# Optimization experiments

Hardware: AMD Instinct MI355X
Metric: run time of the kernel (lower is better)

## Reference

```python
import jax, jax.numpy as jnp
import numpy as np

R, C, N, E = 1, 4, 10000, 160000
H, EF, L, OUT = 128, 16, 3, 64


def _gelu(v):
    # torch F.gelu default = exact erf gelu
    return jax.nn.gelu(v, approximate=False)


def setup_inputs() -> dict:
    key = jax.random.key(0)
    ks = jax.random.split(key, 16)
    s = 0.05
    return {
        "x": jax.random.normal(ks[0], (R, C, N, H), jnp.float32),
        "node_mask": jax.random.uniform(ks[1], (R, C, N, 1), jnp.float32),
        "edge_attr": jax.random.normal(ks[2], (E, EF), jnp.float32),
        "bondW": jax.random.normal(ks[3], (EF, H), jnp.float32) * s,
        "bondb": jnp.zeros((H,), jnp.float32),
        "convW1": jax.random.normal(ks[4], (L, H, H), jnp.float32) * s,
        "convb1": jnp.zeros((L, H), jnp.float32),
        "convW2": jax.random.normal(ks[5], (L, H, H), jnp.float32) * s,
        "convb2": jnp.zeros((L, H), jnp.float32),
        "eps": jnp.zeros((L,), jnp.float32),
        "mlpW1": jax.random.normal(ks[6], (H, H), jnp.float32) * s,
        "mlpb1": jnp.zeros((H,), jnp.float32),
        "mlpW2": jax.random.normal(ks[7], (H, OUT), jnp.float32) * s,
        "mlpb2": jnp.zeros((OUT,), jnp.float32),
        "edge_index": jax.random.randint(ks[8], (2, E), 0, N, jnp.int32),
        "batch": jnp.zeros((N,), jnp.int32),
    }


def reference(x, node_mask, edge_attr, bondW, bondb, convW1, convb1, convW2, convb2,
              eps, mlpW1, mlpb1, mlpW2, mlpb2, edge_index, batch):
    src, dst = edge_index[0], edge_index[1]
    # shared bond encoder (Linear), broadcast to [1,1,E,H]
    edge_emb = edge_attr @ bondW + bondb                      # [E, H]
    # edge_weight = node_mask gathered at both endpoints      # [R, C, E, 1]
    edge_mask = node_mask[:, :, src, :] * node_mask[:, :, dst, :]
    for l in range(L):
        # gather-add-GELU-weight-scatter message passing
        msg = _gelu(x[:, :, src, :] + edge_emb) * edge_mask   # [R, C, E, H]
        agg = jnp.zeros_like(x).at[:, :, dst, :].add(msg)     # scatter_sum over dst
        h = (1.0 + eps[l]) * x + agg
        # conv mlp: Linear -> GELU -> Linear
        h = _gelu(h @ convW1[l] + convb1[l]) @ convW2[l] + convb2[l]
        h = _gelu(h)  # outer activation (norm=Identity, dropout=0)
        x = x + h     # residual
    # final MLP (num_mlp_layers=2, PyG MLP default relu act)
    y = jax.nn.relu(x @ mlpW1 + mlpb1) @ mlpW2 + mlpb2        # [R, C, N, OUT]
    denom = jax.lax.stop_gradient(node_mask).sum(axis=2)      # [R, C, 1]
    out = (y * node_mask).sum(axis=2) / denom                 # [R, C, OUT]
    return out
```

## Files before the change

kernel.cpp:

```cpp
#include <hip/hip_runtime.h>
#include <hip/hip_bf16.h>
#include <cstddef>
#include <cstdint>

#define NNODES 10000
#define NEDGES 160000
#define NH     128
#define NCOMBO 4
#define NMROWS (NCOMBO * NNODES)
#define FTILE  32
#define HSTR   132
#define SSTR   136
#define FTILES (NMROWS / FTILE)

typedef __attribute__((ext_vector_type(8))) short short8v;
typedef __attribute__((ext_vector_type(4))) float f32x4;

__device__ __forceinline__ float gelu_f(float v) {
    const float u  = v * 0.70710678118654752f;
    float au = __builtin_fabsf(u);
    au = fminf(au, 3.9192f);
    const float t  = __builtin_amdgcn_rcpf(__builtin_fmaf(0.3275911f, au, 1.0f));
    const float e  = __builtin_amdgcn_exp2f(au * au * -1.4426950408889634f);
    float p = __builtin_fmaf(1.061405429f, t, -1.453152027f);
    p = __builtin_fmaf(p, t, 1.421413741f);
    p = __builtin_fmaf(p, t, -0.284496736f);
    p = __builtin_fmaf(p, t, 0.254829592f);
    const float erf_abs = 1.0f - p * t * e;
    const float erf_s   = __builtin_copysignf(erf_abs, v);
    return 0.5f * v * (1.0f + erf_s);
}

__device__ __forceinline__ uint16_t f2bf_rne(float f) {
    const uint32_t x = __float_as_uint(f);
    return (uint16_t)((x + 0x7fffu + ((x >> 16) & 1u)) >> 16);
}

__global__ __launch_bounds__(256) void hist_kernel(const int* __restrict__ ei,
                                                   int* __restrict__ deg) {
    const int e = blockIdx.x * 256 + threadIdx.x;
    if (e < NEDGES) atomicAdd(&deg[ei[NEDGES + e]], 1);
}

__global__ __launch_bounds__(1024) void scan_kernel(const int* __restrict__ deg,
                                                    int* __restrict__ off,
                                                    int* __restrict__ cursor) {
    __shared__ int ssum[1024];
    const int tid  = threadIdx.x;
    const int base = tid * 10;
    int loc[10];
    int s = 0;
    #pragma unroll
    for (int i = 0; i < 10; ++i) {
        const int idx = base + i;
        loc[i] = s;
        s += (idx < NNODES) ? deg[idx] : 0;
    }
    ssum[tid] = s;
    for (int d = 1; d < 1024; d <<= 1) {
        __syncthreads();
        const int t = (tid >= d) ? ssum[tid - d] : 0;
        __syncthreads();
        ssum[tid] += t;
    }
    __syncthreads();
    const int pref = ssum[tid] - s;
    #pragma unroll
    for (int i = 0; i < 10; ++i) {
        const int idx = base + i;
        if (idx < NNODES) { off[idx] = pref + loc[i]; cursor[idx] = pref + loc[i]; }
    }
    if (tid == 0) off[NNODES] = NEDGES;
}

__global__ __launch_bounds__(256) void scatter_kernel(const int* __restrict__ ei,
                                                      const float* __restrict__ ea,
                                                      int* __restrict__ cursor,
                                                      int* __restrict__ esrc,
                                                      float* __restrict__ ea_s) {
    const int e = blockIdx.x * 256 + threadIdx.x;
    if (e < NEDGES) {
        const int src = ei[e];
        const int dst = ei[NEDGES + e];
        const int pos = atomicAdd(&cursor[dst], 1);
        esrc[pos] = src;
        const float4* s = reinterpret_cast<const float4*>(ea + (size_t)e * 16);
        float4*       d = reinterpret_cast<float4*>(ea_s + (size_t)pos * 16);
        d[0] = s[0]; d[1] = s[1]; d[2] = s[2]; d[3] = s[3];
    }
}

__global__ __launch_bounds__(256) void emb_kernel(
    const float* __restrict__ ea_s, const float* __restrict__ bW,
    const float* __restrict__ bb, uint32_t* __restrict__ embq)
{
    const int lane = threadIdx.x & 63;
    const int wid  = threadIdx.x >> 6;
    const int c0   = lane * 2;
    float2 wc[16];
    #pragma unroll
    for (int k = 0; k < 16; ++k)
        wc[k] = *reinterpret_cast<const float2*>(&bW[k * 128 + c0]);
    const float2 bbr = *reinterpret_cast<const float2*>(&bb[c0]);

    for (int j = blockIdx.x * 4 + wid; j < NEDGES; j += gridDim.x * 4) {
        const float4* eap = reinterpret_cast<const float4*>(ea_s + (size_t)j * 16);
        const float4 a0 = eap[0], a1 = eap[1], a2 = eap[2], a3 = eap[3];
        float s0 = bbr.x, s1 = bbr.y;
        s0 += a0.x*wc[0].x + a0.y*wc[1].x + a0.z*wc[2].x + a0.w*wc[3].x
            + a1.x*wc[4].x + a1.y*wc[5].x + a1.z*wc[6].x + a1.w*wc[7].x
            + a2.x*wc[8].x + a2.y*wc[9].x + a2.z*wc[10].x + a2.w*wc[11].x
            + a3.x*wc[12].x + a3.y*wc[13].x + a3.z*wc[14].x + a3.w*wc[15].x;
        s1 += a0.x*wc[0].y + a0.y*wc[1].y + a0.z*wc[2].y + a0.w*wc[3].y
            + a1.x*wc[4].y + a1.y*wc[5].y + a1.z*wc[6].y + a1.w*wc[7].y
            + a2.x*wc[8].y + a2.y*wc[9].y + a2.z*wc[10].y + a2.w*wc[11].y
            + a3.x*wc[12].y + a3.y*wc[13].y + a3.z*wc[14].y + a3.w*wc[15].y;
        embq[(size_t)j * 64 + lane] =
            ((uint32_t)f2bf_rne(s1) << 16) | (uint32_t)f2bf_rne(s0);
    }
}

__global__ __launch_bounds__(256) void wtrans_kernel(
    const float* __restrict__ cW1, const float* __restrict__ cW2,
    short* __restrict__ wbf)
{
    const int gidx = blockIdx.x * 256 + threadIdx.x;
    const int m    = gidx >> 14;
    const int el   = gidx & 16383;
    const int n    = el >> 7;
    const int k    = el & 127;
    const float* W = (m < 3) ? (cW1 + m * 16384) : (cW2 + (m - 3) * 16384);
    wbf[(size_t)m * 16384 + n * 128 + k] = (short)f2bf_rne(W[k * 128 + n]);
}

__global__ __launch_bounds__(256) void agg2_kernel(
    const float* __restrict__ xsrc, const float* __restrict__ nm,
    const uint32_t* __restrict__ embq, const int* __restrict__ off,
    const int* __restrict__ esrc, const float* __restrict__ epsp, int layer,
    float* __restrict__ hout)
{
    const int lane = threadIdx.x & 63;
    const int wid  = threadIdx.x >> 6;
    const int c0   = lane * 2;
    const float epv = 1.0f + epsp[layer];

    for (int n = blockIdx.x * 4 + wid; n < NNODES; n += gridDim.x * 4) {
        const int j0 = off[n], j1 = off[n + 1];
        float dm[4];
        #pragma unroll
        for (int c = 0; c < 4; ++c) dm[c] = nm[c * NNODES + n];

        float acc[4][2] = {{0.f,0.f},{0.f,0.f},{0.f,0.f},{0.f,0.f}};

        uint32_t eq_c = 0; float mv_c[4]; float2 xv_c[4];
        if (j0 < j1) {
            const int s = esrc[j0];
            eq_c = embq[(size_t)j0 * 64 + lane];
            #pragma unroll
            for (int c = 0; c < 4; ++c) {
                mv_c[c] = nm[c * NNODES + s] * dm[c];
                xv_c[c] = *reinterpret_cast<const float2*>(
                              &xsrc[((size_t)c * NNODES + s) * NH + c0]);
            }
        }
        for (int j = j0; j < j1; ++j) {
            const uint32_t eq = eq_c;
            float mv[4]; float2 xv[4];
            #pragma unroll
            for (int c = 0; c < 4; ++c) { mv[c] = mv_c[c]; xv[c] = xv_c[c]; }
            if (j + 1 < j1) {
                const int s = esrc[j + 1];
                eq_c = embq[(size_t)(j + 1) * 64 + lane];
                #pragma unroll
                for (int c = 0; c < 4; ++c) {
                    mv_c[c] = nm[c * NNODES + s] * dm[c];
                    xv_c[c] = *reinterpret_cast<const float2*>(
                                  &xsrc[((size_t)c * NNODES + s) * NH + c0]);
                }
            }
            const float e0 = __uint_as_float(eq << 16);
            const float e1 = __uint_as_float(eq & 0xffff0000u);
            #pragma unroll
            for (int c = 0; c < 4; ++c) {
                acc[c][0] += gelu_f(xv[c].x + e0) * mv[c];
                acc[c][1] += gelu_f(xv[c].y + e1) * mv[c];
            }
        }
        #pragma unroll
        for (int c = 0; c < 4; ++c) {
            const float2 xo = *reinterpret_cast<const float2*>(
                                  &xsrc[((size_t)c * NNODES + n) * NH + c0]);
            float2 o;
            o.x = epv * xo.x + acc[c][0];
            o.y = epv * xo.y + acc[c][1];
            *reinterpret_cast<float2*>(&hout[((size_t)c * NNODES + n) * NH + c0]) = o;
        }
    }
}

__global__ __launch_bounds__(256) void agg_kernel(
    const float* __restrict__ xcur, const float* __restrict__ nm,
    const float* __restrict__ ea_s, const float* __restrict__ bW,
    const float* __restrict__ bb, const int* __restrict__ off,
    const int* __restrict__ esrc, const float* __restrict__ epsp, int layer,
    float* __restrict__ hout)
{
    const int tid = threadIdx.x;
    const int h   = tid & 127;
    const int sub = tid >> 7;
    float wc[16];
    #pragma unroll
    for (int k = 0; k < 16; ++k) wc[k] = bW[k * 128 + h];
    const float bbr = bb[h];
    const float epv = 1.0f + epsp[layer];

    for (int n = blockIdx.x * 2 + sub; n < NNODES; n += gridDim.x * 2) {
        float acc0 = 0.f, acc1 = 0.f, acc2 = 0.f, acc3 = 0.f;
        const int j0 = off[n], j1 = off[n + 1];
        const float d0 = nm[0*NNODES+n], d1 = nm[1*NNODES+n];
        const float d2 = nm[2*NNODES+n], d3 = nm[3*NNODES+n];
        for (int j = j0; j < j1; ++j) {
            const int src = esrc[j];
            const float4* eap = reinterpret_cast<const float4*>(ea_s + (size_t)j * 16);
            const float4 a0 = eap[0], a1 = eap[1], a2 = eap[2], a3 = eap[3];
            float emb = bbr;
            emb += a0.x*wc[0] + a0.y*wc[1] + a0.z*wc[2] + a0.w*wc[3];
            emb += a1.x*wc[4] + a1.y*wc[5] + a1.z*wc[6] + a1.w*wc[7];
            emb += a2.x*wc[8] + a2.y*wc[9] + a2.z*wc[10] + a2.w*wc[11];
            emb += a3.x*wc[12] + a3.y*wc[13] + a3.z*wc[14] + a3.w*wc[15];
            const float m0 = nm[0*NNODES+src]*d0, m1 = nm[1*NNODES+src]*d1;
            const float m2 = nm[2*NNODES+src]*d2, m3 = nm[3*NNODES+src]*d3;
            acc0 += gelu_f(xcur[((size_t)0*NNODES+src)*NH+h] + emb) * m0;
            acc1 += gelu_f(xcur[((size_t)1*NNODES+src)*NH+h] + emb) * m1;
            acc2 += gelu_f(xcur[((size_t)2*NNODES+src)*NH+h] + emb) * m2;
            acc3 += gelu_f(xcur[((size_t)3*NNODES+src)*NH+h] + emb) * m3;
        }
        hout[((size_t)0*NNODES+n)*NH+h] = epv * xcur[((size_t)0*NNODES+n)*NH+h] + acc0;
        hout[((size_t)1*NNODES+n)*NH+h] = epv * xcur[((size_t)1*NNODES+n)*NH+h] + acc1;
        hout[((size_t)2*NNODES+n)*NH+h] = epv * xcur[((size_t)2*NNODES+n)*NH+h] + acc2;
        hout[((size_t)3*NNODES+n)*NH+h] = epv * xcur[((size_t)3*NNODES+n)*NH+h] + acc3;
    }
}

__global__ __launch_bounds__(256) void conv_mfma_kernel(
    const float* __restrict__ h,
    const float* __restrict__ resid,
    const short* __restrict__ W1t,
    const float* __restrict__ b1,
    const short* __restrict__ W2t,
    const float* __restrict__ b2,
    float* __restrict__ outp)
{
    __shared__ short sh[FTILE * SSTR];
    __shared__ short st[FTILE * SSTR];
    __shared__ short sw[128 * SSTR];

    const int tid  = threadIdx.x;
    const int lane = tid & 63;
    const int w    = tid >> 6;
    const int l15  = lane & 15;
    const int l4   = lane >> 4;
    const int colb = w * 32;
    const int row0 = blockIdx.x * FTILE;

    for (int i = tid; i < FTILE * 32; i += 256) {
        const int r = i >> 5, q = i & 31;
        const float4 v = reinterpret_cast<const float4*>(h + (size_t)(row0 + r) * NH)[q];
        uint2 pk;
        pk.x = ((uint32_t)f2bf_rne(v.y) << 16) | (uint32_t)f2bf_rne(v.x);
        pk.y = ((uint32_t)f2bf_rne(v.w) << 16) | (uint32_t)f2bf_rne(v.z);
        *reinterpret_cast<uint2*>(&sh[r * SSTR + q * 4]) = pk;
    }
    for (int i = tid; i < 128 * 16; i += 256) {
        const int r = i >> 4, c = i & 15;
        *reinterpret_cast<uint4*>(&sw[r * SSTR + c * 8]) =
            *reinterpret_cast<const uint4*>(&W1t[r * 128 + c * 8]);
    }
    __syncthreads();

    f32x4 a00 = {0,0,0,0}, a01 = {0,0,0,0}, a10 = {0,0,0,0}, a11 = {0,0,0,0};
    #pragma unroll
    for (int s = 0; s < 4; ++s) {
        const int ko = s * 32 + l4 * 8;
        short8v fa0 = *reinterpret_cast<const short8v*>(&sh[(l15)      * SSTR + ko]);
        short8v fa1 = *reinterpret_cast<const short8v*>(&sh[(16 + l15) * SSTR + ko]);
        short8v fb0 = *reinterpret_cast<const short8v*>(&sw[(colb + l15)      * SSTR + ko]);
        short8v fb1 = *reinterpret_cast<const short8v*>(&sw[(colb + 16 + l15) * SSTR + ko]);
        a00 = __builtin_amdgcn_mfma_f32_16x16x32_bf16(fa0, fb0, a00, 0, 0, 0);
        a01 = __builtin_amdgcn_mfma_f32_16x16x32_bf16(fa0, fb1, a01, 0, 0, 0);
        a10 = __builtin_amdgcn_mfma_f32_16x16x32_bf16(fa1, fb0, a10, 0, 0, 0);
        a11 = __builtin_amdgcn_mfma_f32_16x16x32_bf16(fa1, fb1, a11, 0, 0, 0);
    }

    {
        const float bv0 = b1[colb + l15];
        const float bv1 = b1[colb + 16 + l15];
        #pragma unroll
        for (int j = 0; j < 4; ++j) {
            const int r0 = l4 * 4 + j;
            st[r0 * SSTR + colb + l15]           = (short)f2bf_rne(gelu_f(a00[j] + bv0));
            st[r0 * SSTR + colb + 16 + l15]      = (short)f2bf_rne(gelu_f(a01[j] + bv1));
            st[(16 + r0) * SSTR + colb + l15]    = (short)f2bf_rne(gelu_f(a10[j] + bv0));
            st[(16 + r0) * SSTR + colb + 16 + l15] = (short)f2bf_rne(gelu_f(a11[j] + bv1));
        }
    }
    __syncthreads();

    for (int i = tid; i < 128 * 16; i += 256) {
        const int r = i >> 4, c = i & 15;
        *reinterpret_cast<uint4*>(&sw[r * SSTR + c * 8]) =
            *reinterpret_cast<const uint4*>(&W2t[r * 128 + c * 8]);
    }
    __syncthreads();

    a00 = {0,0,0,0}; a01 = {0,0,0,0}; a10 = {0,0,0,0}; a11 = {0,0,0,0};
    #pragma unroll
    for (int s = 0; s < 4; ++s) {
        const int ko = s * 32 + l4 * 8;
        short8v fa0 = *reinterpret_cast<const short8v*>(&st[(l15)      * SSTR + ko]);
        short8v fa1 = *reinterpret_cast<const short8v*>(&st[(16 + l15) * SSTR + ko]);
        short8v fb0 = *reinterpret_cast<const short8v*>(&sw[(colb + l15)      * SSTR + ko]);
        short8v fb1 = *reinterpret_cast<const short8v*>(&sw[(colb + 16 + l15) * SSTR + ko]);
        a00 = __builtin_amdgcn_mfma_f32_16x16x32_bf16(fa0, fb0, a00, 0, 0, 0);
        a01 = __builtin_amdgcn_mfma_f32_16x16x32_bf16(fa0, fb1, a01, 0, 0, 0);
        a10 = __builtin_amdgcn_mfma_f32_16x16x32_bf16(fa1, fb0, a10, 0, 0, 0);
        a11 = __builtin_amdgcn_mfma_f32_16x16x32_bf16(fa1, fb1, a11, 0, 0, 0);
    }

    {
        const float bv0 = b2[colb + l15];
        const float bv1 = b2[colb + 16 + l15];
        #pragma unroll
        for (int j = 0; j < 4; ++j) {
            const int r0 = row0 + l4 * 4 + j;
            const int r1 = r0 + 16;
            const size_t o00 = (size_t)r0 * NH + colb + l15;
            const size_t o01 = (size_t)r0 * NH + colb + 16 + l15;
            const size_t o10 = (size_t)r1 * NH + colb + l15;
            const size_t o11 = (size_t)r1 * NH + colb + 16 + l15;
            outp[o00] = resid[o00] + gelu_f(a00[j] + bv0);
            outp[o01] = resid[o01] + gelu_f(a01[j] + bv1);
            outp[o10] = resid[o10] + gelu_f(a10[j] + bv0);
            outp[o11] = resid[o11] + gelu_f(a11[j] + bv1);
        }
    }
}

__global__ __launch_bounds__(256) void mlp_fused_kernel(
    const float* __restrict__ x,
    const float* __restrict__ W1, const float* __restrict__ b1,
    const float* __restrict__ W2, const float* __restrict__ b2,
    const float* __restrict__ nm, float* __restrict__ oacc)
{
    __shared__ float sh[FTILE * HSTR];
    __shared__ float st[FTILE * HSTR];
    __shared__ float sW[64 * 128];
    __shared__ float sacc[256];

    const int tid = threadIdx.x;
    const int cg  = tid & 31;
    const int ns  = tid >> 5;
    const int ch  = cg * 4;
    const int cg2 = tid & 15;
    const int ns2 = tid >> 4;
    const int ch2 = cg2 * 4;

    sacc[tid] = 0.0f;

    for (int tile = blockIdx.x; tile < FTILES; tile += gridDim.x) {
        const int row0 = tile * FTILE;
        __syncthreads();

        for (int i = tid; i < FTILE * 32; i += 256) {
            const int r  = i >> 5;
            const int kq = i & 31;
            *reinterpret_cast<float4*>(&sh[r * HSTR + kq * 4]) =
                reinterpret_cast<const float4*>(x + (size_t)(row0 + r) * NH)[kq];
        }

        float acc[4][4];
        #pragma unroll
        for (int t = 0; t < 4; ++t) {
            acc[t][0] = 0.f; acc[t][1] = 0.f; acc[t][2] = 0.f; acc[t][3] = 0.f;
        }

        for (int kb = 0; kb < 2; ++kb) {
            __syncthreads();
            const float* Wk = W1 + kb * 64 * 128;
            for (int i = tid * 4; i < 64 * 128; i += 1024)
                *reinterpret_cast<float4*>(&sW[i]) = *reinterpret_cast<const float4*>(Wk + i);
            __syncthreads();

            for (int k = 0; k < 64; ++k) {
                const float4 w = *reinterpret_cast<const float4*>(&sW[k * 128 + ch]);
                #pragma unroll
                for (int t = 0; t < 4; ++t) {
                    const float hv = sh[(ns * 4 + t) * HSTR + kb * 64 + k];
                    acc[t][0] += hv * w.x; acc[t][1] += hv * w.y;
                    acc[t][2] += hv * w.z; acc[t][3] += hv * w.w;
                }
            }
        }

        {
            const float4 bv = *reinterpret_cast<const float4*>(&b1[ch]);
            #pragma unroll
            for (int t = 0; t < 4; ++t) {
                float4 o;
                o.x = fmaxf(acc[t][0] + bv.x, 0.f); o.y = fmaxf(acc[t][1] + bv.y, 0.f);
                o.z = fmaxf(acc[t][2] + bv.z, 0.f); o.w = fmaxf(acc[t][3] + bv.w, 0.f);
                *reinterpret_cast<float4*>(&st[(ns * 4 + t) * HSTR + ch]) = o;
            }
        }

        __syncthreads();
        for (int i = tid * 4; i < 128 * 64; i += 1024)
            *reinterpret_cast<float4*>(&sW[i]) = *reinterpret_cast<const float4*>(W2 + i);
        __syncthreads();

        float a2[2][4];
        a2[0][0]=0.f;a2[0][1]=0.f;a2[0][2]=0.f;a2[0][3]=0.f;
        a2[1][0]=0.f;a2[1][1]=0.f;a2[1][2]=0.f;a2[1][3]=0.f;
        for (int k = 0; k < 128; ++k) {
            const float4 w = *reinterpret_cast<const float4*>(&sW[k * 64 + ch2]);
            #pragma unroll
            for (int t = 0; t < 2; ++t) {
                const float tv = st[(ns2 * 2 + t) * HSTR + k];
                a2[t][0] += tv * w.x; a2[t][1] += tv * w.y;
                a2[t][2] += tv * w.z; a2[t][3] += tv * w.w;
            }
        }

        {
            const float4 bv = *reinterpret_cast<const float4*>(&b2[ch2]);
            #pragma unroll
            for (int t = 0; t < 2; ++t) {
                const int gr = row0 + ns2 * 2 + t;
                const float wgt = nm[gr];
                const int c = gr / NNODES;
                atomicAdd(&sacc[c * 64 + ch2 + 0], (a2[t][0] + bv.x) * wgt);
                atomicAdd(&sacc[c * 64 + ch2 + 1], (a2[t][1] + bv.y) * wgt);
                atomicAdd(&sacc[c * 64 + ch2 + 2], (a2[t][2] + bv.z) * wgt);
                atomicAdd(&sacc[c * 64 + ch2 + 3], (a2[t][3] + bv.w) * wgt);
            }
        }
    }

    __syncthreads();
    atomicAdd(&oacc[tid], sacc[tid]);
}

__global__ __launch_bounds__(256) void final_kernel(
    const float* __restrict__ acc, const float* __restrict__ nm,
    float* __restrict__ outp)
{
    const int tid  = threadIdx.x;
    const int c    = tid >> 6;
    const int lane = tid & 63;
    float s = 0.f;
    for (int n = lane; n < NNODES; n += 64) s += nm[c * NNODES + n];
    #pragma unroll
    for (int off = 32; off > 0; off >>= 1) s += __shfl_down(s, off, 64);
    const float denom = __shfl(s, 0, 64);
    outp[tid] = acc[tid] / denom;
}

extern "C" void kernel_launch(void* const* d_in, const int* in_sizes, int n_in,
                              void* d_out, int out_size, void* d_ws, size_t ws_size,
                              hipStream_t stream) {
    const float* x    = (const float*)d_in[0];
    const float* nm   = (const float*)d_in[1];
    const float* ea   = (const float*)d_in[2];
    const float* bW   = (const float*)d_in[3];
    const float* bb   = (const float*)d_in[4];
    const float* cW1  = (const float*)d_in[5];
    const float* cb1  = (const float*)d_in[6];
    const float* cW2  = (const float*)d_in[7];
    const float* cb2  = (const float*)d_in[8];
    const float* eps  = (const float*)d_in[9];
    const float* mW1  = (const float*)d_in[10];
    const float* mb1  = (const float*)d_in[11];
    const float* mW2  = (const float*)d_in[12];
    const float* mb2  = (const float*)d_in[13];
    const int*   ei   = (const int*)d_in[14];

    float* ws = (float*)d_ws;
    const bool big = ws_size >= (size_t)23230260ULL * 4ULL;

    if (big) {
        float*    xcur = ws;
        float*    hbuf = ws + 5120000;
        float*    oacc = ws + 10240000;
        float*    ea_s = ws + 10240256;
        short*    wbf  = (short*)ea_s;
        uint32_t* embq = (uint32_t*)(ws + 12800256);
        int*      ib   = (int*)(ws + 23040256);
        int* off = ib; int* cur = ib + 10002; int* deg = ib + 20002;
        int* esrc = ib + 30002;

        hipMemsetAsync(deg, 0, 10000 * 4, stream);
        hist_kernel<<<(NEDGES + 255) / 256, 256, 0, stream>>>(ei, deg);
        scan_kernel<<<1, 1024, 0, stream>>>(deg, off, cur);
        scatter_kernel<<<(NEDGES + 255) / 256, 256, 0, stream>>>(ei, ea, cur, esrc, ea_s);
        emb_kernel<<<10000, 256, 0, stream>>>(ea_s, bW, bb, embq);
        wtrans_kernel<<<384, 256, 0, stream>>>(cW1, cW2, wbf);

        for (int l = 0; l < 3; ++l) {
            const float* xs = (l == 0) ? x : xcur;
            agg2_kernel<<<2500, 256, 0, stream>>>(xs, nm, embq, off, esrc, eps, l, hbuf);
            conv_mfma_kernel<<<FTILES, 256, 0, stream>>>(hbuf, xs,
                wbf + (size_t)l * 16384, cb1 + l * 128,
                wbf + (size_t)(3 + l) * 16384, cb2 + l * 128, xcur);
        }
        hipMemsetAsync(oacc, 0, 256 * 4, stream);
        mlp_fused_kernel<<<FTILES, 256, 0, stream>>>(xcur, mW1, mb1, mW2, mb2, nm, oacc);
        final_kernel<<<1, 256, 0, stream>>>(oacc, nm, (float*)d_out);
    } else {
        float* xcur = ws;
        float* hbuf = ws + 5120000;
        float* oacc = ws + 10240000;
        float* ea_s = ws + 10240256;
        int*   ib   = (int*)(ws + 12800256);
        int* off = ib; int* cur = ib + 10002; int* deg = ib + 20002;
        int* esrc = ib + 30002;
        short* wbf = (short*)(ib + 190004);

        hipMemsetAsync(deg, 0, 10000 * 4, stream);
        hist_kernel<<<(NEDGES + 255) / 256, 256, 0, stream>>>(ei, deg);
        scan_kernel<<<1, 1024, 0, stream>>>(deg, off, cur);
        scatter_kernel<<<(NEDGES + 255) / 256, 256, 0, stream>>>(ei, ea, cur, esrc, ea_s);
        wtrans_kernel<<<384, 256, 0, stream>>>(cW1, cW2, wbf);

        for (int l = 0; l < 3; ++l) {
            const float* xs = (l == 0) ? x : xcur;
            agg_kernel<<<2500, 256, 0, stream>>>(xs, nm, ea_s, bW, bb, off, esrc,
                                                 eps, l, hbuf);
            conv_mfma_kernel<<<FTILES, 256, 0, stream>>>(hbuf, xs,
                wbf + (size_t)l * 16384, cb1 + l * 128,
                wbf + (size_t)(3 + l) * 16384, cb2 + l * 128, xcur);
        }
        hipMemsetAsync(oacc, 0, 256 * 4, stream);
        mlp_fused_kernel<<<FTILES, 256, 0, stream>>>(xcur, mW1, mb1, mW2, mb2, nm, oacc);
        final_kernel<<<1, 256, 0, stream>>>(oacc, nm, (float*)d_out);
    }
}
```

Measured before the change: 458.2 us.

## Port final MLP to bf16 MFMA and deepen edge prefetch in aggregation

The final two-layer MLP moves from scalar fp32 FMA loops to bf16 MFMA tiles. Its weights are pre-transposed and converted by the extended weight-transform kernel, which now also handles mW1 and mW2. Separately, the aggregation loop switches from single-buffer to double-buffer prefetching, loading two edges ahead to hide gather latency. The costs are bf16 rounding in the final MLP and higher register pressure in the aggregation kernel. The small-workspace path reuses the wbf offsets, so its layout needs to hold the extra weights.

```diff
diff --git a/kernel.cpp b/kernel.cpp
--- a/kernel.cpp
+++ b/kernel.cpp
@@ -9,7 +9,6 @@
 #define NCOMBO 4
 #define NMROWS (NCOMBO * NNODES)
 #define FTILE  32
-#define HSTR   132
 #define SSTR   136
 #define FTILES (NMROWS / FTILE)
 
@@ -122,15 +121,25 @@
 
 __global__ __launch_bounds__(256) void wtrans_kernel(
     const float* __restrict__ cW1, const float* __restrict__ cW2,
+    const float* __restrict__ mW1, const float* __restrict__ mW2,
     short* __restrict__ wbf)
 {
     const int gidx = blockIdx.x * 256 + threadIdx.x;
-    const int m    = gidx >> 14;
-    const int el   = gidx & 16383;
-    const int n    = el >> 7;
-    const int k    = el & 127;
-    const float* W = (m < 3) ? (cW1 + m * 16384) : (cW2 + (m - 3) * 16384);
-    wbf[(size_t)m * 16384 + n * 128 + k] = (short)f2bf_rne(W[k * 128 + n]);
+    if (gidx >= 122880) return;
+    if (gidx < 114688) {
+        const int m  = gidx >> 14;
+        const int el = gidx & 16383;
+        const int n  = el >> 7;
+        const int k  = el & 127;
+        const float* W = (m < 3) ? (cW1 + m * 16384)
+                       : (m < 6) ? (cW2 + (m - 3) * 16384) : mW1;
+        wbf[(size_t)m * 16384 + n * 128 + k] = (short)f2bf_rne(W[k * 128 + n]);
+    } else {
+        const int el = gidx - 114688;
+        const int n  = el >> 7;
+        const int k  = el & 127;
+        wbf[114688 + n * 128 + k] = (short)f2bf_rne(mW2[k * 64 + n]);
+    }
 }
 
 __global__ __launch_bounds__(256) void agg2_kernel(
@@ -152,40 +161,46 @@
 
         float acc[4][2] = {{0.f,0.f},{0.f,0.f},{0.f,0.f},{0.f,0.f}};
 
-        uint32_t eq_c = 0; float mv_c[4]; float2 xv_c[4];
-        if (j0 < j1) {
-            const int s = esrc[j0];
-            eq_c = embq[(size_t)j0 * 64 + lane];
-            #pragma unroll
-            for (int c = 0; c < 4; ++c) {
-                mv_c[c] = nm[c * NNODES + s] * dm[c];
-                xv_c[c] = *reinterpret_cast<const float2*>(
-                              &xsrc[((size_t)c * NNODES + s) * NH + c0]);
-            }
-        }
-        for (int j = j0; j < j1; ++j) {
-            const uint32_t eq = eq_c;
-            float mv[4]; float2 xv[4];
-            #pragma unroll
-            for (int c = 0; c < 4; ++c) { mv[c] = mv_c[c]; xv[c] = xv_c[c]; }
-            if (j + 1 < j1) {
-                const int s = esrc[j + 1];
-                eq_c = embq[(size_t)(j + 1) * 64 + lane];
-                #pragma unroll
-                for (int c = 0; c < 4; ++c) {
-                    mv_c[c] = nm[c * NNODES + s] * dm[c];
-                    xv_c[c] = *reinterpret_cast<const float2*>(
-                                  &xsrc[((size_t)c * NNODES + s) * NH + c0]);
-                }
-            }
-            const float e0 = __uint_as_float(eq << 16);
-            const float e1 = __uint_as_float(eq & 0xffff0000u);
-            #pragma unroll
-            for (int c = 0; c < 4; ++c) {
-                acc[c][0] += gelu_f(xv[c].x + e0) * mv[c];
-                acc[c][1] += gelu_f(xv[c].y + e1) * mv[c];
-            }
-        }
+        uint32_t eqA = 0, eqB = 0;
+        float mvA[4], mvB[4]; float2 xvA[4], xvB[4];
+
+#define PF(EQ, MV, XV, JJ)                                                   \
+        {                                                                    \
+            const int s_ = esrc[(JJ)];                                       \
+            EQ = embq[(size_t)(JJ) * 64 + lane];                             \
+            _Pragma("unroll")                                                \
+            for (int c = 0; c < 4; ++c) {                                    \
+                MV[c] = nm[c * NNODES + s_] * dm[c];                         \
+                XV[c] = *reinterpret_cast<const float2*>(                    \
+                            &xsrc[((size_t)c * NNODES + s_) * NH + c0]);     \
+            }                                                                \
+        }
+#define CONSUME(EQ, MV, XV)                                                  \
+        {                                                                    \
+            const float e0_ = __uint_as_float(EQ << 16);                     \
+            const float e1_ = __uint_as_float(EQ & 0xffff0000u);             \
+            _Pragma("unroll")                                                \
+            for (int c = 0; c < 4; ++c) {                                    \
+                acc[c][0] += gelu_f(XV[c].x + e0_) * MV[c];                  \
+                acc[c][1] += gelu_f(XV[c].y + e1_) * MV[c];                  \
+            }                                                                \
+        }
+
+        if (j0 < j1)     PF(eqA, mvA, xvA, j0);
+        if (j0 + 1 < j1) PF(eqB, mvB, xvB, j0 + 1);
+        int j = j0;
+        while (j < j1) {
+            CONSUME(eqA, mvA, xvA);
+            if (j + 2 < j1) PF(eqA, mvA, xvA, j + 2);
+            ++j;
+            if (j >= j1) break;
+            CONSUME(eqB, mvB, xvB);
+            if (j + 2 < j1) PF(eqB, mvB, xvB, j + 2);
+            ++j;
+        }
+#undef PF
+#undef CONSUME
+
         #pragma unroll
         for (int c = 0; c < 4; ++c) {
             const float2 xo = *reinterpret_cast<const float2*>(
@@ -243,12 +258,9 @@
 }
 
 __global__ __launch_bounds__(256) void conv_mfma_kernel(
-    const float* __restrict__ h,
-    const float* __restrict__ resid,
-    const short* __restrict__ W1t,
-    const float* __restrict__ b1,
-    const short* __restrict__ W2t,
-    const float* __restrict__ b2,
+    const float* __restrict__ h, const float* __restrict__ resid,
+    const short* __restrict__ W1t, const float* __restrict__ b1,
+    const short* __restrict__ W2t, const float* __restrict__ b2,
     float* __restrict__ outp)
 {
     __shared__ short sh[FTILE * SSTR];
@@ -298,9 +310,9 @@
         #pragma unroll
         for (int j = 0; j < 4; ++j) {
             const int r0 = l4 * 4 + j;
-            st[r0 * SSTR + colb + l15]           = (short)f2bf_rne(gelu_f(a00[j] + bv0));
-            st[r0 * SSTR + colb + 16 + l15]      = (short)f2bf_rne(gelu_f(a01[j] + bv1));
-            st[(16 + r0) * SSTR + colb + l15]    = (short)f2bf_rne(gelu_f(a10[j] + bv0));
+            st[r0 * SSTR + colb + l15]             = (short)f2bf_rne(gelu_f(a00[j] + bv0));
+            st[r0 * SSTR + colb + 16 + l15]        = (short)f2bf_rne(gelu_f(a01[j] + bv1));
+            st[(16 + r0) * SSTR + colb + l15]      = (short)f2bf_rne(gelu_f(a10[j] + bv0));
             st[(16 + r0) * SSTR + colb + 16 + l15] = (short)f2bf_rne(gelu_f(a11[j] + bv1));
         }
     }
@@ -346,103 +358,103 @@
     }
 }
 
-__global__ __launch_bounds__(256) void mlp_fused_kernel(
+__global__ __launch_bounds__(256) void mlp_mfma_kernel(
     const float* __restrict__ x,
-    const float* __restrict__ W1, const float* __restrict__ b1,
-    const float* __restrict__ W2, const float* __restrict__ b2,
-    const float* __restrict__ nm, float* __restrict__ oacc)
-{
-    __shared__ float sh[FTILE * HSTR];
-    __shared__ float st[FTILE * HSTR];
-    __shared__ float sW[64 * 128];
+    const short* __restrict__ W1t, const float* __restrict__ b1,
+    const short* __restrict__ W2t,
+    const float* __restrict__ b2,
+    const float* __restrict__ nm,
+    float* __restrict__ oacc)
+{
+    __shared__ short sx[FTILE * SSTR];
+    __shared__ short st[FTILE * SSTR];
+    __shared__ short sw[128 * SSTR];
     __shared__ float sacc[256];
 
-    const int tid = threadIdx.x;
-    const int cg  = tid & 31;
-    const int ns  = tid >> 5;
-    const int ch  = cg * 4;
-    const int cg2 = tid & 15;
-    const int ns2 = tid >> 4;
-    const int ch2 = cg2 * 4;
+    const int tid  = threadIdx.x;
+    const int lane = tid & 63;
+    const int w    = tid >> 6;
+    const int l15  = lane & 15;
+    const int l4   = lane >> 4;
+    const int colb = w * 32;
+    const int row0 = blockIdx.x * FTILE;
 
     sacc[tid] = 0.0f;
 
-    for (int tile = blockIdx.x; tile < FTILES; tile += gridDim.x) {
-        const int row0 = tile * FTILE;
-        __syncthreads();
-
-        for (int i = tid; i < FTILE * 32; i += 256) {
-            const int r  = i >> 5;
-            const int kq = i & 31;
-            *reinterpret_cast<float4*>(&sh[r * HSTR + kq * 4]) =
-                reinterpret_cast<const float4*>(x + (size_t)(row0 + r) * NH)[kq];
-        }
-
-        float acc[4][4];
+    for (int i = tid; i < FTILE * 32; i += 256) {
+        const int r = i >> 5, q = i & 31;
+        const float4 v = reinterpret_cast<const float4*>(x + (size_t)(row0 + r) * NH)[q];
+        uint2 pk;
+        pk.x = ((uint32_t)f2bf_rne(v.y) << 16) | (uint32_t)f2bf_rne(v.x);
+        pk.y = ((uint32_t)f2bf_rne(v.w) << 16) | (uint32_t)f2bf_rne(v.z);
+        *reinterpret_cast<uint2*>(&sx[r * SSTR + q * 4]) = pk;
+    }
+    for (int i = tid; i < 128 * 16; i += 256) {
+        const int r = i >> 4, c = i & 15;
+        *reinterpret_cast<uint4*>(&sw[r * SSTR + c * 8]) =
+            *reinterpret_cast<const uint4*>(&W1t[r * 128 + c * 8]);
+    }
+    __syncthreads();
+
+    f32x4 a00 = {0,0,0,0}, a01 = {0,0,0,0}, a10 = {0,0,0,0}, a11 = {0,0,0,0};
+    #pragma unroll
+    for (int s = 0; s < 4; ++s) {
+        const int ko = s * 32 + l4 * 8;
+        short8v fa0 = *reinterpret_cast<const short8v*>(&sx[(l15)      * SSTR + ko]);
+        short8v fa1 = *reinterpret_cast<const short8v*>(&sx[(16 + l15) * SSTR + ko]);
+        short8v fb0 = *reinterpret_cast<const short8v*>(&sw[(colb + l15)      * SSTR + ko]);
+        short8v fb1 = *reinterpret_cast<const short8v*>(&sw[(colb + 16 + l15) * SSTR + ko]);
+        a00 = __builtin_amdgcn_mfma_f32_16x16x32_bf16(fa0, fb0, a00, 0, 0, 0);
+        a01 = __builtin_amdgcn_mfma_f32_16x16x32_bf16(fa0, fb1, a01, 0, 0, 0);
+        a10 = __builtin_amdgcn_mfma_f32_16x16x32_bf16(fa1, fb0, a10, 0, 0, 0);
+        a11 = __builtin_amdgcn_mfma_f32_16x16x32_bf16(fa1, fb1, a11, 0, 0, 0);
+    }
+
+    {
+        const float bv0 = b1[colb + l15];
+        const float bv1 = b1[colb + 16 + l15];
         #pragma unroll
-        for (int t = 0; t < 4; ++t) {
-            acc[t][0] = 0.f; acc[t][1] = 0.f; acc[t][2] = 0.f; acc[t][3] = 0.f;
-        }
-
-        for (int kb = 0; kb < 2; ++kb) {
-            __syncthreads();
-            const float* Wk = W1 + kb * 64 * 128;
-            for (int i = tid * 4; i < 64 * 128; i += 1024)
-                *reinterpret_cast<float4*>(&sW[i]) = *reinterpret_cast<const float4*>(Wk + i);
-            __syncthreads();
-
-            for (int k = 0; k < 64; ++k) {
-                const float4 w = *reinterpret_cast<const float4*>(&sW[k * 128 + ch]);
-                #pragma unroll
-                for (int t = 0; t < 4; ++t) {
-                    const float hv = sh[(ns * 4 + t) * HSTR + kb * 64 + k];
-                    acc[t][0] += hv * w.x; acc[t][1] += hv * w.y;
-                    acc[t][2] += hv * w.z; acc[t][3] += hv * w.w;
-                }
-            }
-        }
-
-        {
-            const float4 bv = *reinterpret_cast<const float4*>(&b1[ch]);
-            #pragma unroll
-            for (int t = 0; t < 4; ++t) {
-                float4 o;
-                o.x = fmaxf(acc[t][0] + bv.x, 0.f); o.y = fmaxf(acc[t][1] + bv.y, 0.f);
-                o.z = fmaxf(acc[t][2] + bv.z, 0.f); o.w = fmaxf(acc[t][3] + bv.w, 0.f);
-                *reinterpret_cast<float4*>(&st[(ns * 4 + t) * HSTR + ch]) = o;
-            }
-        }
-
-        __syncthreads();
-        for (int i = tid * 4; i < 128 * 64; i += 1024)
-            *reinterpret_cast<float4*>(&sW[i]) = *reinterpret_cast<const float4*>(W2 + i);
-        __syncthreads();
-
-        float a2[2][4];
-        a2[0][0]=0.f;a2[0][1]=0.f;a2[0][2]=0.f;a2[0][3]=0.f;
-        a2[1][0]=0.f;a2[1][1]=0.f;a2[1][2]=0.f;a2[1][3]=0.f;
-        for (int k = 0; k < 128; ++k) {
-            const float4 w = *reinterpret_cast<const float4*>(&sW[k * 64 + ch2]);
-            #pragma unroll
-            for (int t = 0; t < 2; ++t) {
-                const float tv = st[(ns2 * 2 + t) * HSTR + k];
-                a2[t][0] += tv * w.x; a2[t][1] += tv * w.y;
-                a2[t][2] += tv * w.z; a2[t][3] += tv * w.w;
-            }
-        }
-
-        {
-            const float4 bv = *reinterpret_cast<const float4*>(&b2[ch2]);
-            #pragma unroll
-            for (int t = 0; t < 2; ++t) {
-                const int gr = row0 + ns2 * 2 + t;
-                const float wgt = nm[gr];
-                const int c = gr / NNODES;
-                atomicAdd(&sacc[c * 64 + ch2 + 0], (a2[t][0] + bv.x) * wgt);
-                atomicAdd(&sacc[c * 64 + ch2 + 1], (a2[t][1] + bv.y) * wgt);
-                atomicAdd(&sacc[c * 64 + ch2 + 2], (a2[t][2] + bv.z) * wgt);
-                atomicAdd(&sacc[c * 64 + ch2 + 3], (a2[t][3] + bv.w) * wgt);
-            }
+        for (int j = 0; j < 4; ++j) {
+            const int r0 = l4 * 4 + j;
+            st[r0 * SSTR + colb + l15]             = (short)f2bf_rne(fmaxf(a00[j] + bv0, 0.f));
+            st[r0 * SSTR + colb + 16 + l15]        = (short)f2bf_rne(fmaxf(a01[j] + bv1, 0.f));
+            st[(16 + r0) * SSTR + colb + l15]      = (short)f2bf_rne(fmaxf(a10[j] + bv0, 0.f));
+            st[(16 + r0) * SSTR + colb + 16 + l15] = (short)f2bf_rne(fmaxf(a11[j] + bv1, 0.f));
+        }
+    }
+    __syncthreads();
+
+    for (int i = tid; i < 64 * 16; i += 256) {
+        const int r = i >> 4, c = i & 15;
+        *reinterpret_cast<uint4*>(&sw[r * SSTR + c * 8]) =
+            *reinterpret_cast<const uint4*>(&W2t[r * 128 + c * 8]);
+    }
+    __syncthreads();
+
+    const int colb2 = w * 16;
+    f32x4 c0f = {0,0,0,0}, c1f = {0,0,0,0};
+    #pragma unroll
+    for (int s = 0; s < 4; ++s) {
+        const int ko = s * 32 + l4 * 8;
+        short8v fa0 = *reinterpret_cast<const short8v*>(&st[(l15)      * SSTR + ko]);
+        short8v fa1 = *reinterpret_cast<const short8v*>(&st[(16 + l15) * SSTR + ko]);
+        short8v fb  = *reinterpret_cast<const short8v*>(&sw[(colb2 + l15) * SSTR + ko]);
+        c0f = __builtin_amdgcn_mfma_f32_16x16x32_bf16(fa0, fb, c0f, 0, 0, 0);
+        c1f = __builtin_amdgcn_mfma_f32_16x16x32_bf16(fa1, fb, c1f, 0, 0, 0);
+    }
+
+    {
+        const float bv = b2[colb2 + l15];
+        #pragma unroll
+        for (int j = 0; j < 4; ++j) {
+            const int gr0 = row0 + l4 * 4 + j;
+            const int gr1 = gr0 + 16;
+            const float w0 = nm[gr0];
+            const float w1 = nm[gr1];
+            const int cb0 = gr0 / NNODES;
+            const int cb1 = gr1 / NNODES;
+            atomicAdd(&sacc[cb0 * 64 + colb2 + l15], (c0f[j] + bv) * w0);
+            atomicAdd(&sacc[cb1 * 64 + colb2 + l15], (c1f[j] + bv) * w1);
         }
     }
 
@@ -503,7 +515,7 @@
         scan_kernel<<<1, 1024, 0, stream>>>(deg, off, cur);
         scatter_kernel<<<(NEDGES + 255) / 256, 256, 0, stream>>>(ei, ea, cur, esrc, ea_s);
         emb_kernel<<<10000, 256, 0, stream>>>(ea_s, bW, bb, embq);
-        wtrans_kernel<<<384, 256, 0, stream>>>(cW1, cW2, wbf);
+        wtrans_kernel<<<480, 256, 0, stream>>>(cW1, cW2, mW1, mW2, wbf);
 
         for (int l = 0; l < 3; ++l) {
             const float* xs = (l == 0) ? x : xcur;
@@ -513,7 +525,8 @@
                 wbf + (size_t)(3 + l) * 16384, cb2 + l * 128, xcur);
         }
         hipMemsetAsync(oacc, 0, 256 * 4, stream);
-        mlp_fused_kernel<<<FTILES, 256, 0, stream>>>(xcur, mW1, mb1, mW2, mb2, nm, oacc);
+        mlp_mfma_kernel<<<FTILES, 256, 0, stream>>>(xcur, wbf + 98304, mb1,
+                                                    wbf + 114688, mb2, nm, oacc);
         final_kernel<<<1, 256, 0, stream>>>(oacc, nm, (float*)d_out);
     } else {
         float* xcur = ws;
@@ -529,7 +542,7 @@
         hist_kernel<<<(NEDGES + 255) / 256, 256, 0, stream>>>(ei, deg);
         scan_kernel<<<1, 1024, 0, stream>>>(deg, off, cur);
         scatter_kernel<<<(NEDGES + 255) / 256, 256, 0, stream>>>(ei, ea, cur, esrc, ea_s);
-        wtrans_kernel<<<384, 256, 0, stream>>>(cW1, cW2, wbf);
+        wtrans_kernel<<<480, 256, 0, stream>>>(cW1, cW2, mW1, mW2, wbf);
 
         for (int l = 0; l < 3; ++l) {
             const float* xs = (l == 0) ? x : xcur;
@@ -540,7 +553,8 @@
                 wbf + (size_t)(3 + l) * 16384, cb2 + l * 128, xcur);
         }
         hipMemsetAsync(oacc, 0, 256 * 4, stream);
-        mlp_fused_kernel<<<FTILES, 256, 0, stream>>>(xcur, mW1, mb1, mW2, mb2, nm, oacc);
+        mlp_mfma_kernel<<<FTILES, 256, 0, stream>>>(xcur, wbf + 98304, mb1,
+                                                    wbf + 114688, mb2, nm, oacc);
         final_kernel<<<1, 256, 0, stream>>>(oacc, nm, (float*)d_out);
     }
 }
```

After: 452.4 us. No clear change (-1.2%).
